# Optimization experiments

Hardware: AMD Instinct MI355X
Metric: run time of the kernel (lower is better)

## Reference

```python
import jax, jax.numpy as jnp
import numpy as np

B, CIN, COUT, N, R = 4, 32, 64, 65536, 32
PAD = 0.1
NEG_SLOPE = 0.1


def _norm_coords(coords):
    # coords [B,3,N] in [-1,1]; map to continuous voxel space [0, R-1]
    return jnp.clip((coords / (1.0 + PAD) + 1.0) * 0.5 * (R - 1), 0.0, R - 1)


def scatter_mean(feat, coords):
    # feat [B,C,N], coords [B,3,N] -> voxel grid [B,C,R,R,R]
    b, c, n = feat.shape
    nc = _norm_coords(coords)
    idx = jnp.clip(jnp.floor(nc + 0.5), 0, R - 1).astype(jnp.int32)  # nearest voxel
    flat = (idx[:, 0] * R + idx[:, 1]) * R + idx[:, 2]               # [B,N]
    seg = (flat + jnp.arange(b, dtype=jnp.int32)[:, None] * (R ** 3)).reshape(-1)
    f = feat.transpose(0, 2, 1).reshape(b * n, c)
    sums = jax.ops.segment_sum(f, seg, num_segments=b * R ** 3)
    cnt = jax.ops.segment_sum(jnp.ones((b * n,), feat.dtype), seg, num_segments=b * R ** 3)
    mean = sums / jnp.maximum(cnt, 1.0)[:, None]
    return mean.reshape(b, R, R, R, c).transpose(0, 4, 1, 2, 3)


def trilinear_sample(grid, coords):
    # grid [B,C,R,R,R], coords [B,3,N] -> point features [B,C,N]
    b, c = grid.shape[:2]
    n = coords.shape[-1]
    nc = _norm_coords(coords)                      # [B,3,N]
    lo = jnp.floor(nc).astype(jnp.int32)
    lo = jnp.clip(lo, 0, R - 1)
    hi = jnp.minimum(lo + 1, R - 1)
    frac = nc - lo.astype(nc.dtype)                # [B,3,N]
    gflat = grid.reshape(b, c, R ** 3).transpose(0, 2, 1)  # [B, R^3, C]

    def corner(ix, iy, iz):
        fi = (ix * R + iy) * R + iz                # [B,N]
        return jnp.take_along_axis(gflat, fi[..., None], axis=1)  # [B,N,C]

    fx, fy, fz = frac[:, 0], frac[:, 1], frac[:, 2]
    x0, y0, z0 = lo[:, 0], lo[:, 1], lo[:, 2]
    x1, y1, z1 = hi[:, 0], hi[:, 1], hi[:, 2]
    w = lambda a: a[..., None]
    out = (corner(x0, y0, z0) * w((1 - fx) * (1 - fy) * (1 - fz))
           + corner(x0, y0, z1) * w((1 - fx) * (1 - fy) * fz)
           + corner(x0, y1, z0) * w((1 - fx) * fy * (1 - fz))
           + corner(x0, y1, z1) * w((1 - fx) * fy * fz)
           + corner(x1, y0, z0) * w(fx * (1 - fy) * (1 - fz))
           + corner(x1, y0, z1) * w(fx * (1 - fy) * fz)
           + corner(x1, y1, z0) * w(fx * fy * (1 - fz))
           + corner(x1, y1, z1) * w(fx * fy * fz))
    return out.transpose(0, 2, 1)                  # [B,C,N]


def conv3d(x, w, b):
    y = jax.lax.conv_general_dilated(x, w, (1, 1, 1), 'SAME',
                                     dimension_numbers=('NCDHW', 'OIDHW', 'NCDHW'))
    return y + b[None, :, None, None, None]


def leaky(x):
    return jnp.where(x >= 0, x, NEG_SLOPE * x)


def setup_inputs() -> dict:
    key = jax.random.key(0)
    ks = jax.random.split(key, 6)
    features = jax.random.normal(ks[0], (B, CIN, N), jnp.float32)
    inputs = jax.random.uniform(ks[1], (B, 3, N), jnp.float32) * 2.0 - 1.0  # coords in [-1,1]
    w_mlp = jax.random.normal(ks[2], (COUT, CIN), jnp.float32) * 0.05
    b_mlp = jnp.zeros((COUT,), jnp.float32)
    w_conv1 = jax.random.normal(ks[3], (COUT, CIN, 3, 3, 3), jnp.float32) * 0.05
    b_conv1 = jnp.zeros((COUT,), jnp.float32)
    w_conv2 = jax.random.normal(ks[4], (COUT, COUT, 3, 3, 3), jnp.float32) * 0.05
    b_conv2 = jnp.zeros((COUT,), jnp.float32)
    return {"features": features, "inputs": inputs, "w_mlp": w_mlp, "b_mlp": b_mlp,
            "w_conv1": w_conv1, "b_conv1": b_conv1, "w_conv2": w_conv2, "b_conv2": b_conv2}


def reference(features, inputs, w_mlp, b_mlp, w_conv1, b_conv1, w_conv2, b_conv2):
    # First PVConv layer: voxelize point features (scatter-mean)
    voxel_in = scatter_mean(features, inputs)                     # [B,CIN,R,R,R]
    # point branch: Conv1d(k=1) + ReLU (mlp=False path, norm=None)
    point_feature = jax.nn.relu(jnp.einsum('oc,bcn->bon', w_mlp, features) + b_mlp[None, :, None])
    # voxel branch: DoubleConv = (conv3d -> leaky_relu) x 2, layer_order 'cna' with norm=None
    v = leaky(conv3d(voxel_in, w_conv1, b_conv1))
    voxel_feature = leaky(conv3d(v, w_conv2, b_conv2))            # [B,COUT,R,R,R]
    # fuse point feature: trilinear devoxelization gather + add
    sampled = trilinear_sample(voxel_feature, inputs)             # [B,COUT,N]
    point_out = point_feature + sampled
    return (point_out, voxel_feature)
```

## Files before the change

### kernel.cpp

```cpp
#include <hip/hip_runtime.h>

typedef unsigned short ushort_t;
typedef unsigned int uint_t;
typedef __attribute__((ext_vector_type(4))) float f32x4;
typedef __attribute__((ext_vector_type(16))) float f32x16;
typedef __attribute__((ext_vector_type(4))) unsigned int u32x4;
typedef __attribute__((ext_vector_type(8))) short short8;

#define R3 32768
#define NPTS 65536

__device__ __forceinline__ float bf_lo(uint_t u) { return __uint_as_float(u << 16); }
__device__ __forceinline__ float bf_hi(uint_t u) { return __uint_as_float(u & 0xffff0000u); }
__device__ __forceinline__ ushort_t f2b(float f) {
    uint_t u = __float_as_uint(f);
    u += 0x7fffu + ((u >> 16) & 1u);
    return (ushort_t)(u >> 16);
}
__device__ __forceinline__ float normc(float c) {
    float v = (c / 1.1f + 1.0f) * 0.5f * 31.0f;
    return fminf(fmaxf(v, 0.0f), 31.0f);
}

__device__ __forceinline__ void gload16(const ushort_t* g, ushort_t* l) {
    __builtin_amdgcn_global_load_lds(
        (const __attribute__((address_space(1))) unsigned int*)g,
        (__attribute__((address_space(3))) unsigned int*)l, 16, 0, 0);
}

__global__ __launch_bounds__(256) void k_vid(const float* __restrict__ coords,
                                             int* __restrict__ vid,
                                             uint_t* __restrict__ hist) {
    int gid = blockIdx.x * 256 + threadIdx.x;
    int b = gid >> 16, n = gid & 65535;
    const float* cp = coords + (size_t)b * 3 * NPTS + n;
    int ix = (int)floorf(normc(cp[0]) + 0.5f);
    int iy = (int)floorf(normc(cp[NPTS]) + 0.5f);
    int iz = (int)floorf(normc(cp[2 * NPTS]) + 0.5f);
    ix = min(max(ix, 0), 31); iy = min(max(iy, 0), 31); iz = min(max(iz, 0), 31);
    int v = b * R3 + ((ix * 32 + iy) * 32 + iz);
    vid[gid] = v;
    atomicAdd(hist + v, 1u);
}

__global__ __launch_bounds__(256) void k_scanA(const uint_t* __restrict__ hist,
                                               uint_t* __restrict__ excl,
                                               uint_t* __restrict__ bsum) {
    __shared__ uint_t sh[256];
    int t = threadIdx.x;
    int base = blockIdx.x * 1024 + t * 4;
    uint_t v0 = hist[base], v1 = hist[base + 1], v2 = hist[base + 2], v3 = hist[base + 3];
    uint_t s = v0 + v1 + v2 + v3;
    sh[t] = s;
    __syncthreads();
    uint_t x = s;
    for (int off = 1; off < 256; off <<= 1) {
        uint_t y = (t >= off) ? sh[t - off] : 0u;
        __syncthreads();
        x += y;
        sh[t] = x;
        __syncthreads();
    }
    uint_t e = x - s;
    excl[base] = e;
    excl[base + 1] = e + v0;
    excl[base + 2] = e + v0 + v1;
    excl[base + 3] = e + v0 + v1 + v2;
    if (t == 255) bsum[blockIdx.x] = x;
}

__global__ __launch_bounds__(128) void k_scanB(uint_t* __restrict__ bsum,
                                               uint_t* __restrict__ boff) {
    __shared__ uint_t sh[128];
    int t = threadIdx.x;
    uint_t s = bsum[t];
    sh[t] = s;
    __syncthreads();
    uint_t x = s;
    for (int off = 1; off < 128; off <<= 1) {
        uint_t y = (t >= off) ? sh[t - off] : 0u;
        __syncthreads();
        x += y;
        sh[t] = x;
        __syncthreads();
    }
    boff[t] = x - s;
}

__global__ __launch_bounds__(256) void k_scanC(uint_t* __restrict__ excl,
                                               const uint_t* __restrict__ boff,
                                               uint_t* __restrict__ cursor) {
    int i = blockIdx.x * 256 + threadIdx.x;
    uint_t v = excl[i] + boff[i >> 10];
    excl[i] = v;
    cursor[i] = v;
}

__global__ __launch_bounds__(256) void k_scatfeat(const float* __restrict__ feat,
                                                  const int* __restrict__ vid,
                                                  uint_t* __restrict__ cursor,
                                                  ushort_t* __restrict__ sorted) {
    int gid = blockIdx.x * 256 + threadIdx.x;
    int b = gid >> 16, n = gid & 65535;
    int v = vid[gid];
    uint_t slot = atomicAdd(cursor + v, 1u);
    const float* f = feat + (size_t)b * 32 * NPTS + n;
    ushort_t* dst = sorted + (size_t)slot * 32;
#pragma unroll
    for (int q = 0; q < 4; ++q) {
        u32x4 val;
#pragma unroll
        for (int j = 0; j < 4; ++j) {
            float a = f[(size_t)(q * 8 + j * 2) * NPTS];
            float c = f[(size_t)(q * 8 + j * 2 + 1) * NPTS];
            val[j] = (uint_t)f2b(a) | ((uint_t)f2b(c) << 16);
        }
        *(u32x4*)(dst + q * 8) = val;
    }
}

__global__ __launch_bounds__(256) void k_reduce(const ushort_t* __restrict__ sorted,
                                                const uint_t* __restrict__ start,
                                                const uint_t* __restrict__ hist,
                                                ushort_t* __restrict__ mean_cl) {
    int v = blockIdx.x * 256 + threadIdx.x;
    uint_t s = start[v], c = hist[v];
    float acc[32];
#pragma unroll
    for (int i = 0; i < 32; ++i) acc[i] = 0.0f;
    for (uint_t i = 0; i < c; ++i) {
        const u32x4* p = (const u32x4*)(sorted + (size_t)(s + i) * 32);
#pragma unroll
        for (int q = 0; q < 4; ++q) {
            u32x4 val = p[q];
#pragma unroll
            for (int j = 0; j < 4; ++j) {
                acc[q * 8 + j * 2] += bf_lo(val[j]);
                acc[q * 8 + j * 2 + 1] += bf_hi(val[j]);
            }
        }
    }
    float inv = 1.0f / fmaxf((float)c, 1.0f);
    ushort_t* dst = mean_cl + (size_t)v * 32;
#pragma unroll
    for (int q = 0; q < 4; ++q) {
        u32x4 val;
#pragma unroll
        for (int j = 0; j < 4; ++j)
            val[j] = (uint_t)f2b(acc[q * 8 + j * 2] * inv) |
                     ((uint_t)f2b(acc[q * 8 + j * 2 + 1] * inv) << 16);
        *(u32x4*)(dst + q * 8) = val;
    }
}

__global__ __launch_bounds__(256) void k_wpack(const float* __restrict__ w1,
                                               const float* __restrict__ w2,
                                               ushort_t* __restrict__ Wp1,
                                               ushort_t* __restrict__ Wp2) {
    int t = blockIdx.x * 256 + threadIdx.x;
    if (t < 55296) {
        int dz = t / 18432, r = t % 18432;
        int kb = r >> 9, o = (r >> 3) & 63, ke = r & 7;
        int k = kb * 8 + ke, ci = k & 31, n9 = k >> 5;
        Wp1[t] = f2b(w1[(o * 32 + ci) * 27 + n9 * 3 + dz]);
    } else if (t < 165888) {
        int u = t - 55296;
        int dz = u / 36864, r = u % 36864;
        int kb = r >> 9, o = (r >> 3) & 63, ke = r & 7;
        int k = kb * 8 + ke, ci = k & 63, n9 = k >> 6;
        Wp2[u] = f2b(w2[(o * 64 + ci) * 27 + n9 * 3 + dz]);
    }
}

template <int CB, bool WRITE_CF>
__global__ __launch_bounds__(256) void k_conv(const ushort_t* __restrict__ in_b16,
                                              const ushort_t* __restrict__ Wp,
                                              const float* __restrict__ bias,
                                              const ushort_t* __restrict__ zpage,
                                              ushort_t* __restrict__ out_cl,
                                              float* __restrict__ out_cf) {
    constexpr int CI = CB * 8;
    constexpr int CHUNKS = CB * 10 * 19;
    constexpr int CPW = (CHUNKS + 255) / 256;
    constexpr int CHUNKS_PAD = CPW * 256;
    __shared__ union ShU {
        ushort_t T[CHUNKS_PAD * 8];
        float S[64][133];
    } sh;
    int tid = threadIdx.x, bid = blockIdx.x;
    int zh = bid & 1, ys = (bid >> 1) & 3, x = (bid >> 3) & 31, b = bid >> 8;
    int y0 = ys * 8, z0 = zh * 16;
    int lane = tid & 63, wv = tid >> 6;

    int soff[CPW];
    bool vld[CPW];
#pragma unroll
    for (int i = 0; i < CPW; ++i) {
        int c = (wv * CPW + i) * 64 + lane;
        int zz = c % 19, t1 = c / 19, yy = t1 % 10, cb = t1 / 10;
        int gy = y0 + yy - 1, gz = z0 + zz - 1;
        vld[i] = (c < CHUNKS) & ((unsigned)gy < 32u) & ((unsigned)gz < 32u);
        soff[i] = (gy * 32 + gz) * CI + cb * 8;
    }
    const ushort_t* inb = in_b16 + (size_t)b * R3 * CI;

    auto stage = [&](int dx) {
        int gx = x + dx - 1;
        bool xok = (unsigned)gx < 32u;
        const ushort_t* base = inb + (size_t)gx * (1024 * CI);
#pragma unroll
        for (int i = 0; i < CPW; ++i) {
            const ushort_t* src = (xok && vld[i]) ? (base + soff[i]) : zpage;
            gload16(src, &sh.T[(wv * CPW + i) * 512]);
        }
    };

    int nq = wv & 1, mq = wv >> 1;
    int l31 = lane & 31, lh = lane >> 5;
    int o = nq * 32 + l31;
    int ya0 = mq * 4 + (l31 >> 4);
    int ya1 = ya0 + 2;
    int za = l31 & 15;

    f32x16 acc0, acc1;
#pragma unroll
    for (int i = 0; i < 16; ++i) { acc0[i] = 0.0f; acc1[i] = 0.0f; }

    stage(0);
    __syncthreads();
#pragma unroll
    for (int dx = 0; dx < 3; ++dx) {
        const ushort_t* Tp = &sh.T[0];
        const ushort_t* wpB = Wp + (size_t)o * 8;
#pragma unroll
        for (int dz = 0; dz < 3; ++dz)
#pragma unroll
            for (int dy = 0; dy < 3; ++dy)
#pragma unroll
                for (int cbp = 0; cbp < CB / 2; ++cbp) {
                    int cb = cbp * 2 + lh;
                    const ushort_t* tb = Tp + (size_t)cb * (10 * 19 * 8);
                    short8 a0 = *(const short8*)(tb + ((ya0 + dy) * 19 + za + dz) * 8);
                    short8 a1 = *(const short8*)(tb + ((ya1 + dy) * 19 + za + dz) * 8);
                    int kb = (dx * 3 + dy) * CB + cb;
                    short8 bw = *(const short8*)(wpB + (size_t)(dz * 9 * CB + kb) * 512);
                    acc0 = __builtin_amdgcn_mfma_f32_32x32x16_bf16(a0, bw, acc0, 0, 0, 0);
                    acc1 = __builtin_amdgcn_mfma_f32_32x32x16_bf16(a1, bw, acc1, 0, 0, 0);
                }
        __syncthreads();
        if (dx < 2) {
            stage(dx + 1);
            __syncthreads();
        }
    }

    float bia = bias[o];
#pragma unroll
    for (int i = 0; i < 2; ++i) {
        int mbase = (mq * 2 + i) * 32 + lh * 4;
#pragma unroll
        for (int rq = 0; rq < 4; ++rq) {
            f32x4 v4;
#pragma unroll
            for (int j = 0; j < 4; ++j) {
                float v = (i ? acc1[rq * 4 + j] : acc0[rq * 4 + j]) + bia;
                v4[j] = (v >= 0.0f) ? v : 0.1f * v;
            }
            *(f32x4*)(&sh.S[o][mbase + rq * 8]) = v4;
        }
    }
    __syncthreads();

    {
        int vl = tid >> 1, oh = tid & 1;
        int y = vl >> 4, z = vl & 15;
        ushort_t* dst =
            out_cl + ((size_t)(b * R3 + x * 1024 + (y0 + y) * 32 + z0 + z)) * 64 + oh * 32;
#pragma unroll
        for (int q = 0; q < 4; ++q) {
            u32x4 w;
#pragma unroll
            for (int j4 = 0; j4 < 4; ++j4) {
                int oo = oh * 32 + q * 8 + j4 * 2;
                w[j4] = (uint_t)f2b(sh.S[oo][vl]) | ((uint_t)f2b(sh.S[oo + 1][vl]) << 16);
            }
            *(u32x4*)(dst + q * 8) = w;
        }
    }
    if (WRITE_CF) {
        int oo = tid >> 2, zq = tid & 3;
        float* dp = out_cf + (size_t)(b * 64 + oo) * R3 + x * 1024 + y0 * 32 + z0 + zq * 4;
#pragma unroll
        for (int y = 0; y < 8; ++y)
            *(f32x4*)(dp + y * 32) = *(const f32x4*)(&sh.S[oo][y * 16 + zq * 4]);
    }
}

__global__ __launch_bounds__(256) void k_point(const float* __restrict__ feat,
                                               const float* __restrict__ coords,
                                               const float* __restrict__ w_mlp,
                                               const float* __restrict__ b_mlp,
                                               const ushort_t* __restrict__ vf,
                                               float* __restrict__ out) {
    __shared__ int vox_s[64][8];
    __shared__ float wgt_s[64][8];
    __shared__ float S[64][65];
    int tid = threadIdx.x;
    int b = blockIdx.x >> 10;
    int p0 = (blockIdx.x & 1023) * 64;

    {
        int p = tid & 63, cpair = tid >> 6;
        const float* cp = coords + (size_t)b * 3 * NPTS + p0 + p;
        float nx = normc(cp[0]), ny = normc(cp[NPTS]), nz = normc(cp[2 * NPTS]);
        int x0 = min(max((int)floorf(nx), 0), 31);
        int y0 = min(max((int)floorf(ny), 0), 31);
        int z0 = min(max((int)floorf(nz), 0), 31);
        float fx = nx - (float)x0, fy = ny - (float)y0, fz = nz - (float)z0;
        int x1 = min(x0 + 1, 31), y1 = min(y0 + 1, 31), z1 = min(z0 + 1, 31);
#pragma unroll
        for (int j = 0; j < 2; ++j) {
            int c = cpair * 2 + j;
            int xi = (c & 4) ? x1 : x0, yi = (c & 2) ? y1 : y0, zi = (c & 1) ? z1 : z0;
            float wc = ((c & 4) ? fx : 1.0f - fx) * ((c & 2) ? fy : 1.0f - fy) *
                       ((c & 1) ? fz : 1.0f - fz);
            vox_s[p][c] = (xi * 32 + yi) * 32 + zi;
            wgt_s[p][c] = wc;
        }
    }
    __syncthreads();

    int lane = tid & 63, wv = tid >> 6;
    {
        const ushort_t* vfb = vf + (size_t)b * R3 * 64 + lane;
        for (int t = 0; t < 16; ++t) {
            int p = wv * 16 + t;
            float s = 0.0f;
#pragma unroll
            for (int c = 0; c < 8; ++c) {
                int vox = vox_s[p][c];
                float wc = wgt_s[p][c];
                uint_t raw = (uint_t)vfb[(size_t)vox * 64];
                s = fmaf(wc, __uint_as_float(raw << 16), s);
            }
            S[p][lane] = s;
        }
    }
    __syncthreads();

    {
        int o0 = __builtin_amdgcn_readfirstlane(wv) * 16;
        const float* fb = feat + (size_t)b * 32 * NPTS + p0 + lane;
        float ft[32];
#pragma unroll
        for (int ci = 0; ci < 32; ++ci) ft[ci] = fb[(size_t)ci * NPTS];
        float* ob = out + ((size_t)b * 64 + o0) * NPTS + p0 + lane;
#pragma unroll
        for (int oi = 0; oi < 16; ++oi) {
            float m = b_mlp[o0 + oi];
            const float* wrow = w_mlp + (size_t)(o0 + oi) * 32;
#pragma unroll
            for (int ci = 0; ci < 32; ++ci) m = fmaf(wrow[ci], ft[ci], m);
            m = fmaxf(m, 0.0f);
            ob[(size_t)oi * NPTS] = m + S[lane][o0 + oi];
        }
    }
}

extern "C" void kernel_launch(void* const* d_in, const int* in_sizes, int n_in,
                              void* d_out, int out_size, void* d_ws, size_t ws_size,
                              hipStream_t stream) {
    const float* feat   = (const float*)d_in[0];
    const float* coords = (const float*)d_in[1];
    const float* w_mlp  = (const float*)d_in[2];
    const float* b_mlp  = (const float*)d_in[3];
    const float* w_c1   = (const float*)d_in[4];
    const float* b_c1   = (const float*)d_in[5];
    const float* w_c2   = (const float*)d_in[6];
    const float* b_c2   = (const float*)d_in[7];

    float* out = (float*)d_out;
    float* point_out = out;
    float* vfeat = out + 16777216;

    ushort_t* sorted  = (ushort_t*)out;
    ushort_t* mean_cl = (ushort_t*)(out + 4194304);
    ushort_t* v_cl    = (ushort_t*)(out + 6291456);
    int*      vid     = (int*)(out + 10485760);
    uint_t*   hist    = (uint_t*)(out + 10747904);
    uint_t*   excl    = (uint_t*)(out + 10878976);
    uint_t*   cursor  = (uint_t*)(out + 11010048);
    uint_t*   bsum    = (uint_t*)(out + 11141120);
    uint_t*   boff    = (uint_t*)(out + 11141248);
    ushort_t* Wp1     = (ushort_t*)(out + 11141376);
    ushort_t* Wp2     = (ushort_t*)(out + 11169024);
    ushort_t* zpage   = (ushort_t*)(out + 11224320);
    ushort_t* vf_cl   = (ushort_t*)d_ws;

    hipMemsetAsync(hist, 0, 131072 * 4, stream);
    hipMemsetAsync(zpage, 0, 256, stream);
    k_wpack<<<648, 256, 0, stream>>>(w_c1, w_c2, Wp1, Wp2);
    k_vid<<<1024, 256, 0, stream>>>(coords, vid, hist);
    k_scanA<<<128, 256, 0, stream>>>(hist, excl, bsum);
    k_scanB<<<1, 128, 0, stream>>>(bsum, boff);
    k_scanC<<<512, 256, 0, stream>>>(excl, boff, cursor);
    k_scatfeat<<<1024, 256, 0, stream>>>(feat, vid, cursor, sorted);
    k_reduce<<<512, 256, 0, stream>>>(sorted, excl, hist, mean_cl);
    k_conv<4, false><<<1024, 256, 0, stream>>>(mean_cl, Wp1, b_c1, zpage, v_cl,
                                               (float*)nullptr);
    k_conv<8, true><<<1024, 256, 0, stream>>>(v_cl, Wp2, b_c2, zpage, vf_cl, vfeat);
    k_point<<<4096, 256, 0, stream>>>(feat, coords, w_mlp, b_mlp, vf_cl, point_out);
}
```

Measured before the change: 197.7 us.

## Prefetch next conv input slab into registers while computing current slab

Replaces the direct global-to-LDS loads in the conv kernel with register-staged loads. The next dx slab is loaded into registers before the MFMA loop and written to LDS after the barrier, so global-memory latency overlaps with compute. The zero page and its memset go away, since out-of-bounds chunks now become zeros in registers. The cost is extra VGPRs for the staging buffer, which the added launch-bounds occupancy hint of 4 may pressure, plus an extra register-to-LDS write pass.

Measured after the change: 166.9 us. -15.6%, faster.

```diff
diff --git a/kernel.cpp b/kernel.cpp
--- a/kernel.cpp
+++ b/kernel.cpp
@@ -20,12 +20,6 @@
 __device__ __forceinline__ float normc(float c) {
     float v = (c / 1.1f + 1.0f) * 0.5f * 31.0f;
     return fminf(fmaxf(v, 0.0f), 31.0f);
-}
-
-__device__ __forceinline__ void gload16(const ushort_t* g, ushort_t* l) {
-    __builtin_amdgcn_global_load_lds(
-        (const __attribute__((address_space(1))) unsigned int*)g,
-        (__attribute__((address_space(3))) unsigned int*)l, 16, 0, 0);
 }
 
 __global__ __launch_bounds__(256) void k_vid(const float* __restrict__ coords,
@@ -173,12 +167,11 @@
 }
 
 template <int CB, bool WRITE_CF>
-__global__ __launch_bounds__(256) void k_conv(const ushort_t* __restrict__ in_b16,
-                                              const ushort_t* __restrict__ Wp,
-                                              const float* __restrict__ bias,
-                                              const ushort_t* __restrict__ zpage,
-                                              ushort_t* __restrict__ out_cl,
-                                              float* __restrict__ out_cf) {
+__global__ __launch_bounds__(256, 4) void k_conv(const ushort_t* __restrict__ in_b16,
+                                                 const ushort_t* __restrict__ Wp,
+                                                 const float* __restrict__ bias,
+                                                 ushort_t* __restrict__ out_cl,
+                                                 float* __restrict__ out_cf) {
     constexpr int CI = CB * 8;
     constexpr int CHUNKS = CB * 10 * 19;
     constexpr int CPW = (CHUNKS + 255) / 256;
@@ -204,15 +197,21 @@
     }
     const ushort_t* inb = in_b16 + (size_t)b * R3 * CI;
 
-    auto stage = [&](int dx) {
+    u32x4 sreg[CPW];
+    auto stage_load = [&](int dx) {
         int gx = x + dx - 1;
         bool xok = (unsigned)gx < 32u;
         const ushort_t* base = inb + (size_t)gx * (1024 * CI);
 #pragma unroll
         for (int i = 0; i < CPW; ++i) {
-            const ushort_t* src = (xok && vld[i]) ? (base + soff[i]) : zpage;
-            gload16(src, &sh.T[(wv * CPW + i) * 512]);
-        }
+            u32x4 z4 = {0u, 0u, 0u, 0u};
+            sreg[i] = (xok && vld[i]) ? *(const u32x4*)(base + soff[i]) : z4;
+        }
+    };
+    auto stage_write = [&]() {
+#pragma unroll
+        for (int i = 0; i < CPW; ++i)
+            *(u32x4*)(&sh.T[((wv * CPW + i) * 64 + lane) * 8]) = sreg[i];
     };
 
     int nq = wv & 1, mq = wv >> 1;
@@ -226,10 +225,12 @@
 #pragma unroll
     for (int i = 0; i < 16; ++i) { acc0[i] = 0.0f; acc1[i] = 0.0f; }
 
-    stage(0);
+    stage_load(0);
+    stage_write();
     __syncthreads();
 #pragma unroll
     for (int dx = 0; dx < 3; ++dx) {
+        if (dx < 2) stage_load(dx + 1);
         const ushort_t* Tp = &sh.T[0];
         const ushort_t* wpB = Wp + (size_t)o * 8;
 #pragma unroll
@@ -249,7 +250,7 @@
                 }
         __syncthreads();
         if (dx < 2) {
-            stage(dx + 1);
+            stage_write();
             __syncthreads();
         }
     }
@@ -394,11 +395,9 @@
     uint_t*   boff    = (uint_t*)(out + 11141248);
     ushort_t* Wp1     = (ushort_t*)(out + 11141376);
     ushort_t* Wp2     = (ushort_t*)(out + 11169024);
-    ushort_t* zpage   = (ushort_t*)(out + 11224320);
     ushort_t* vf_cl   = (ushort_t*)d_ws;
 
     hipMemsetAsync(hist, 0, 131072 * 4, stream);
-    hipMemsetAsync(zpage, 0, 256, stream);
     k_wpack<<<648, 256, 0, stream>>>(w_c1, w_c2, Wp1, Wp2);
     k_vid<<<1024, 256, 0, stream>>>(coords, vid, hist);
     k_scanA<<<128, 256, 0, stream>>>(hist, excl, bsum);
@@ -406,8 +405,7 @@
     k_scanC<<<512, 256, 0, stream>>>(excl, boff, cursor);
     k_scatfeat<<<1024, 256, 0, stream>>>(feat, vid, cursor, sorted);
     k_reduce<<<512, 256, 0, stream>>>(sorted, excl, hist, mean_cl);
-    k_conv<4, false><<<1024, 256, 0, stream>>>(mean_cl, Wp1, b_c1, zpage, v_cl,
-                                               (float*)nullptr);
-    k_conv<8, true><<<1024, 256, 0, stream>>>(v_cl, Wp2, b_c2, zpage, vf_cl, vfeat);
+    k_conv<4, false><<<1024, 256, 0, stream>>>(mean_cl, Wp1, b_c1, v_cl, (float*)nullptr);
+    k_conv<8, true><<<1024, 256, 0, stream>>>(v_cl, Wp2, b_c2, vf_cl, vfeat);
     k_point<<<4096, 256, 0, stream>>>(feat, coords, w_mlp, b_mlp, vf_cl, point_out);
 }
```

## Halve conv3d output tile per block to double grid and raise occupancy

Applied to the files above, without the earlier changes.

The conv kernels now compute an 8x8 (y,z) tile per block instead of 8x16, with one MFMA accumulator per wave instead of two, and launch 2048 blocks instead of 1024. The shared staging buffer and epilogue transpose buffer are shrunk, and the epilogue writes output channels in two halves with extra barriers. A launch-bounds hint of 8 blocks per CU is added. The aim is higher occupancy and more blocks to spread across CUs. The cost is more halo re-staging per output (11 vs 19 z-width for half the outputs), half the MFMA work per staged load, and extra synchronisation.

Result: no change. 196.6 us (-0.6%).

```diff
diff --git a/kernel.cpp b/kernel.cpp
--- a/kernel.cpp
+++ b/kernel.cpp
@@ -173,23 +173,22 @@
 }
 
 template <int CB, bool WRITE_CF>
-__global__ __launch_bounds__(256) void k_conv(const ushort_t* __restrict__ in_b16,
-                                              const ushort_t* __restrict__ Wp,
-                                              const float* __restrict__ bias,
-                                              const ushort_t* __restrict__ zpage,
-                                              ushort_t* __restrict__ out_cl,
-                                              float* __restrict__ out_cf) {
+__global__ __launch_bounds__(256, 8) void k_conv(const ushort_t* __restrict__ in_b16,
+                                                 const ushort_t* __restrict__ Wp,
+                                                 const float* __restrict__ bias,
+                                                 const ushort_t* __restrict__ zpage,
+                                                 ushort_t* __restrict__ out_cl,
+                                                 float* __restrict__ out_cf) {
     constexpr int CI = CB * 8;
-    constexpr int CHUNKS = CB * 10 * 19;
+    constexpr int CHUNKS = CB * 10 * 11;
     constexpr int CPW = (CHUNKS + 255) / 256;
-    constexpr int CHUNKS_PAD = CPW * 256;
     __shared__ union ShU {
-        ushort_t T[CHUNKS_PAD * 8];
-        float S[64][133];
+        ushort_t T[CPW * 256 * 8];
+        float S[32][69];
     } sh;
     int tid = threadIdx.x, bid = blockIdx.x;
-    int zh = bid & 1, ys = (bid >> 1) & 3, x = (bid >> 3) & 31, b = bid >> 8;
-    int y0 = ys * 8, z0 = zh * 16;
+    int zq4 = bid & 3, ys = (bid >> 2) & 3, x = (bid >> 4) & 31, b = bid >> 9;
+    int y0 = ys * 8, z0 = zq4 * 8;
     int lane = tid & 63, wv = tid >> 6;
 
     int soff[CPW];
@@ -197,7 +196,7 @@
 #pragma unroll
     for (int i = 0; i < CPW; ++i) {
         int c = (wv * CPW + i) * 64 + lane;
-        int zz = c % 19, t1 = c / 19, yy = t1 % 10, cb = t1 / 10;
+        int zz = c % 11, t1 = c / 11, yy = t1 % 10, cb = t1 / 10;
         int gy = y0 + yy - 1, gz = z0 + zz - 1;
         vld[i] = (c < CHUNKS) & ((unsigned)gy < 32u) & ((unsigned)gz < 32u);
         soff[i] = (gy * 32 + gz) * CI + cb * 8;
@@ -218,13 +217,12 @@
     int nq = wv & 1, mq = wv >> 1;
     int l31 = lane & 31, lh = lane >> 5;
     int o = nq * 32 + l31;
-    int ya0 = mq * 4 + (l31 >> 4);
-    int ya1 = ya0 + 2;
-    int za = l31 & 15;
-
-    f32x16 acc0, acc1;
-#pragma unroll
-    for (int i = 0; i < 16; ++i) { acc0[i] = 0.0f; acc1[i] = 0.0f; }
+    int ya = mq * 4 + (l31 >> 3);
+    int za = l31 & 7;
+
+    f32x16 acc;
+#pragma unroll
+    for (int i = 0; i < 16; ++i) acc[i] = 0.0f;
 
     stage(0);
     __syncthreads();
@@ -239,13 +237,11 @@
 #pragma unroll
                 for (int cbp = 0; cbp < CB / 2; ++cbp) {
                     int cb = cbp * 2 + lh;
-                    const ushort_t* tb = Tp + (size_t)cb * (10 * 19 * 8);
-                    short8 a0 = *(const short8*)(tb + ((ya0 + dy) * 19 + za + dz) * 8);
-                    short8 a1 = *(const short8*)(tb + ((ya1 + dy) * 19 + za + dz) * 8);
+                    const ushort_t* tb = Tp + (size_t)cb * (10 * 11 * 8);
+                    short8 a = *(const short8*)(tb + ((ya + dy) * 11 + za + dz) * 8);
                     int kb = (dx * 3 + dy) * CB + cb;
                     short8 bw = *(const short8*)(wpB + (size_t)(dz * 9 * CB + kb) * 512);
-                    acc0 = __builtin_amdgcn_mfma_f32_32x32x16_bf16(a0, bw, acc0, 0, 0, 0);
-                    acc1 = __builtin_amdgcn_mfma_f32_32x32x16_bf16(a1, bw, acc1, 0, 0, 0);
+                    acc = __builtin_amdgcn_mfma_f32_32x32x16_bf16(a, bw, acc, 0, 0, 0);
                 }
         __syncthreads();
         if (dx < 2) {
@@ -256,43 +252,48 @@
 
     float bia = bias[o];
 #pragma unroll
-    for (int i = 0; i < 2; ++i) {
-        int mbase = (mq * 2 + i) * 32 + lh * 4;
-#pragma unroll
-        for (int rq = 0; rq < 4; ++rq) {
-            f32x4 v4;
-#pragma unroll
-            for (int j = 0; j < 4; ++j) {
-                float v = (i ? acc1[rq * 4 + j] : acc0[rq * 4 + j]) + bia;
-                v4[j] = (v >= 0.0f) ? v : 0.1f * v;
+    for (int oh = 0; oh < 2; ++oh) {
+        if (nq == oh) {
+#pragma unroll
+            for (int rq = 0; rq < 4; ++rq) {
+                f32x4 v4;
+#pragma unroll
+                for (int j = 0; j < 4; ++j) {
+                    float v = acc[rq * 4 + j] + bia;
+                    v4[j] = (v >= 0.0f) ? v : 0.1f * v;
+                }
+                *(f32x4*)(&sh.S[l31][mq * 32 + lh * 4 + rq * 8]) = v4;
             }
-            *(f32x4*)(&sh.S[o][mbase + rq * 8]) = v4;
-        }
-    }
-    __syncthreads();
-
-    {
-        int vl = tid >> 1, oh = tid & 1;
-        int y = vl >> 4, z = vl & 15;
-        ushort_t* dst =
-            out_cl + ((size_t)(b * R3 + x * 1024 + (y0 + y) * 32 + z0 + z)) * 64 + oh * 32;
-#pragma unroll
-        for (int q = 0; q < 4; ++q) {
+        }
+        __syncthreads();
+        {
+            int vl = tid >> 2, qi = tid & 3;
+            int y = y0 + ((vl >> 5) * 4) + ((vl >> 3) & 3), z = z0 + (vl & 7);
+            ushort_t* dst =
+                out_cl + ((size_t)(b * R3 + x * 1024 + y * 32 + z)) * 64 + oh * 32 + qi * 8;
             u32x4 w;
 #pragma unroll
             for (int j4 = 0; j4 < 4; ++j4) {
-                int oo = oh * 32 + q * 8 + j4 * 2;
-                w[j4] = (uint_t)f2b(sh.S[oo][vl]) | ((uint_t)f2b(sh.S[oo + 1][vl]) << 16);
+                int ol = qi * 8 + j4 * 2;
+                w[j4] = (uint_t)f2b(sh.S[ol][vl]) | ((uint_t)f2b(sh.S[ol + 1][vl]) << 16);
             }
-            *(u32x4*)(dst + q * 8) = w;
-        }
-    }
-    if (WRITE_CF) {
-        int oo = tid >> 2, zq = tid & 3;
-        float* dp = out_cf + (size_t)(b * 64 + oo) * R3 + x * 1024 + y0 * 32 + z0 + zq * 4;
-#pragma unroll
-        for (int y = 0; y < 8; ++y)
-            *(f32x4*)(dp + y * 32) = *(const f32x4*)(&sh.S[oo][y * 16 + zq * 4]);
+            *(u32x4*)dst = w;
+        }
+        if (WRITE_CF) {
+            int ol = tid >> 3, ti = tid & 7;
+            int msub = ti >> 2, yo = ti & 3;
+            float* dp = out_cf + (size_t)(b * 64 + oh * 32 + ol) * R3 + x * 1024 +
+                        (y0 + msub * 4 + yo) * 32 + z0;
+#pragma unroll
+            for (int zq = 0; zq < 2; ++zq) {
+                f32x4 tv;
+#pragma unroll
+                for (int j = 0; j < 4; ++j)
+                    tv[j] = sh.S[ol][msub * 32 + yo * 8 + zq * 4 + j];
+                *(f32x4*)(dp + zq * 4) = tv;
+            }
+        }
+        __syncthreads();
     }
 }
 
@@ -406,8 +407,8 @@
     k_scanC<<<512, 256, 0, stream>>>(excl, boff, cursor);
     k_scatfeat<<<1024, 256, 0, stream>>>(feat, vid, cursor, sorted);
     k_reduce<<<512, 256, 0, stream>>>(sorted, excl, hist, mean_cl);
-    k_conv<4, false><<<1024, 256, 0, stream>>>(mean_cl, Wp1, b_c1, zpage, v_cl,
+    k_conv<4, false><<<2048, 256, 0, stream>>>(mean_cl, Wp1, b_c1, zpage, v_cl,
                                                (float*)nullptr);
-    k_conv<8, true><<<1024, 256, 0, stream>>>(v_cl, Wp2, b_c2, zpage, vf_cl, vfeat);
+    k_conv<8, true><<<2048, 256, 0, stream>>>(v_cl, Wp2, b_c2, zpage, vf_cl, vfeat);
     k_point<<<4096, 256, 0, stream>>>(feat, coords, w_mlp, b_mlp, vf_cl, point_out);
 }
```
